# Performance work log

Measured on AMD Instinct MI355X. Metric: run time of the kernel, lower is better.

The kernel has to match this reference:

```python
import jax, jax.numpy as jnp
import numpy as np

D = 128        # d_model
VOCAB = 2000   # vocab_size
NUM_ITERS = 6
NUM_V = 98304  # total vertices = 3 * num_edges
NUM_E = NUM_V // 3


def setup_inputs() -> dict:
    key = jax.random.key(0)
    ks = jax.random.split(key, 20)
    std = 0.02
    inp = {
        "x_v": jax.random.randint(ks[0], (NUM_V,), 0, VOCAB),
        "target_mask": jax.random.randint(ks[1], (NUM_V,), 0, 2) > 0,
        # embedding table (vocab_size + 1 rows, last is padding idx)
        "emb": jax.random.normal(ks[2], (VOCAB + 1, D), jnp.float32) * std,
        # edge_init: Linear(1, d_model)
        "edge_init_w": jax.random.normal(ks[3], (D, 1), jnp.float32) * std,
        "edge_init_b": jnp.zeros((D,), jnp.float32),
        # vertex_to_edge LSTM(3d -> d): torch gate order i,f,g,o
        "Wih_v2e": jax.random.normal(ks[4], (4 * D, 3 * D), jnp.float32) * (1.0 / np.sqrt(D)),
        "Whh_v2e": jax.random.normal(ks[5], (4 * D, D), jnp.float32) * (1.0 / np.sqrt(D)),
        "bih_v2e": jax.random.normal(ks[6], (4 * D,), jnp.float32) * (1.0 / np.sqrt(D)),
        "bhh_v2e": jax.random.normal(ks[7], (4 * D,), jnp.float32) * (1.0 / np.sqrt(D)),
        # edge_to_vertex: 3 position-specific LSTM(d -> d), stacked along axis 0
        "Wih_e2v": jax.random.normal(ks[8], (3, 4 * D, D), jnp.float32) * (1.0 / np.sqrt(D)),
        "Whh_e2v": jax.random.normal(ks[9], (3, 4 * D, D), jnp.float32) * (1.0 / np.sqrt(D)),
        "bih_e2v": jax.random.normal(ks[10], (3, 4 * D), jnp.float32) * (1.0 / np.sqrt(D)),
        "bhh_e2v": jax.random.normal(ks[11], (3, 4 * D), jnp.float32) * (1.0 / np.sqrt(D)),
        # output projection Linear(d -> vocab)
        "out_w": jax.random.normal(ks[12], (VOCAB, D), jnp.float32) * std,
        "out_b": jnp.zeros((VOCAB,), jnp.float32),
    }
    return inp


def _lstm_cell(gates, c):
    # torch LSTM gate order: input, forget, cell(g), output
    i, f, g, o = jnp.split(gates, 4, axis=-1)
    c_new = jax.nn.sigmoid(f) * c + jax.nn.sigmoid(i) * jnp.tanh(g)
    h_new = jax.nn.sigmoid(o) * jnp.tanh(c_new)
    return h_new, c_new


def reference(x_v, target_mask, emb, edge_init_w, edge_init_b,
              Wih_v2e, Whh_v2e, bih_v2e, bhh_v2e,
              Wih_e2v, Whh_e2v, bih_e2v, bhh_e2v,
              out_w, out_b):
    E = x_v.shape[0] // 3
    # init embeddings (-1 ids would map to padding row VOCAB; ids are in-range here)
    h_v = emb[x_v].reshape(E, 3, D)              # [E, 3, D]
    c_v = jnp.zeros_like(h_v)
    h_e = jnp.broadcast_to(edge_init_w[:, 0] + edge_init_b, (E, D))  # Linear(1->D) on ones
    c_e = jnp.zeros_like(h_e)
    mask = target_mask.reshape(E, 3)[..., None]  # [E, 3, 1]
    b_v2e = bih_v2e + bhh_v2e                    # [4D]
    b_e2v = (bih_e2v + bhh_e2v)[None]            # [1, 3, 4D]

    for _ in range(NUM_ITERS):
        # vertex -> edge: concat 3 vertices, one LSTM cell step
        msg = h_v.reshape(E, 3 * D)
        gates_e = msg @ Wih_v2e.T + h_e @ Whh_v2e.T + b_v2e          # [E, 4D]
        h_e, c_e = _lstm_cell(gates_e, c_e)
        # edge -> vertex: 3 position-specific LSTM cells, same edge input
        gates_v = (jnp.einsum('ed,pkd->epk', h_e, Wih_e2v)
                   + jnp.einsum('epd,pkd->epk', h_v, Whh_e2v)
                   + b_e2v)                                          # [E, 3, 4D]
        h_new, c_new = _lstm_cell(gates_v, c_v)
        h_v = jnp.where(mask, h_new, h_v)
        c_v = jnp.where(mask, c_new, c_v)

    logits = h_v.reshape(3 * E, D) @ out_w.T + out_b                 # [3E, VOCAB]
    return logits
```

## Files before the change

kernel.cpp:

```cpp
#include <hip/hip_runtime.h>

#define E_CNT 32768
#define V_CNT 98304
#define D_ 128
#define VOCAB_ 2000
#define ITERS_ 6

typedef unsigned short u16;
typedef _Float16 f16;
typedef __attribute__((ext_vector_type(8))) _Float16 f16x8;
typedef __attribute__((ext_vector_type(4))) float f32x4;

__device__ __forceinline__ f32x4 MFh(f16x8 a, f16x8 b, f32x4 c) {
    return __builtin_amdgcn_mfma_f32_16x16x32_f16(a, b, c, 0, 0, 0);
}
__device__ __forceinline__ float sigmoid_f(float x) {
    return __builtin_amdgcn_rcpf(1.0f + __expf(-x));
}
__device__ __forceinline__ float tanh_f(float x) {
    float ax = fabsf(x);
    float t = fmaf(-2.0f, __builtin_amdgcn_rcpf(__expf(2.0f * ax) + 1.0f), 1.0f);
    return copysignf(t, x);
}

__global__ void detect_mask_kernel(const unsigned int* __restrict__ m, int* __restrict__ flag) {
    int i = blockIdx.x * 256 + threadIdx.x;
    if (i < 4096 && m[i] > 1u) atomicOr(flag, 1);
}

__global__ void prep_kernel(
    const float* __restrict__ Wih_v2e, const float* __restrict__ Whh_v2e,
    const float* __restrict__ bih_v2e, const float* __restrict__ bhh_v2e,
    const float* __restrict__ Wih_e2v, const float* __restrict__ Whh_e2v,
    const float* __restrict__ bih_e2v, const float* __restrict__ bhh_e2v,
    const float* __restrict__ out_w,
    f16* __restrict__ WvF, f16* __restrict__ WeF, f16* __restrict__ OwF,
    float* __restrict__ bv, float* __restrict__ be)
{
    int idx = blockIdx.x * 256 + threadIdx.x;
    if (idx < 262144) {
        const int r = idx & 7, l = (idx >> 3) & 63, t = idx >> 9;
        const int kk = t & 15, nt = t >> 4;
        const int j = nt * 16 + (l & 15);
        const int k = kk * 32 + (l >> 4) * 8 + r;
        const float w = (k < 384) ? Wih_v2e[j * 384 + k] : Whh_v2e[j * 128 + (k - 384)];
        WvF[idx] = (f16)w;
        return;
    }
    idx -= 262144;
    if (idx < 393216) {
        const int r = idx & 7, l = (idx >> 3) & 63, t = idx >> 9;
        const int kk = t & 7, nt = (t >> 3) & 31, p = t >> 8;
        const int j = nt * 16 + (l & 15);
        const int k = kk * 32 + (l >> 4) * 8 + r;
        const float w = (k < 128) ? Wih_e2v[(p * 512 + j) * 128 + k]
                                  : Whh_e2v[(p * 512 + j) * 128 + (k - 128)];
        WeF[idx] = (f16)w;
        return;
    }
    idx -= 393216;
    if (idx < 256000) {
        const int r = idx & 7, l = (idx >> 3) & 63, t = idx >> 9;
        const int kk = t & 3, nt = t >> 2;
        const int j = nt * 16 + (l & 15);
        const int k = kk * 32 + (l >> 4) * 8 + r;
        OwF[idx] = (f16)out_w[j * 128 + k];
        return;
    }
    idx -= 256000;
    if (idx < 512) { bv[idx] = bih_v2e[idx] + bhh_v2e[idx]; return; }
    idx -= 512;
    if (idx < 1536) { be[idx] = bih_e2v[idx] + bhh_e2v[idx]; return; }
}

__global__ __launch_bounds__(512)
void fused_kernel(
    const int* __restrict__ x_v,
    const float* __restrict__ emb,
    const float* __restrict__ eiw, const float* __restrict__ eib,
    const f16* __restrict__ WvF, const f16* __restrict__ WeF,
    const float* __restrict__ bv, const float* __restrict__ be,
    const void* __restrict__ mask, const int* __restrict__ flagp,
    float4* __restrict__ cvG4,
    f16* __restrict__ hvOut)
{
    __shared__ f16 HV[24576];
    __shared__ f16 HE[8192];

    const int tid = threadIdx.x;
    const int c = tid >> 6, l = tid & 63;
    const int lr = l & 15, lk = l >> 4;
    const int e0 = blockIdx.x * 64;

    for (int i = tid; i < 64 * 48; i += 512) {
        const int row = i / 48, seg = i % 48;
        int id = x_v[(e0 + row) * 3 + (seg >> 4)];
        if (id < 0 || id > VOCAB_) id = VOCAB_;
        const float* s = emb + id * D_ + ((seg * 8) & 127);
        float4 a = *(const float4*)s, b = *(const float4*)(s + 4);
        f16x8 H;
        H[0] = (f16)a.x; H[1] = (f16)a.y; H[2] = (f16)a.z; H[3] = (f16)a.w;
        H[4] = (f16)b.x; H[5] = (f16)b.y; H[6] = (f16)b.z; H[7] = (f16)b.w;
        *(f16x8*)&HV[((row >> 4) * 12 + (seg >> 2)) * 512 + (seg & 3) * 128 + (row & 15) * 8] = H;
    }
    for (int i = tid; i < 64 * 16; i += 512) {
        const int row = i / 16, seg = i % 16;
        f16x8 H;
        #pragma unroll
        for (int j = 0; j < 8; ++j) H[j] = (f16)(eiw[seg * 8 + j] + eib[seg * 8 + j]);
        *(f16x8*)&HE[((row >> 4) * 4 + (seg >> 2)) * 512 + (seg & 3) * 128 + (row & 15) * 8] = H;
    }

    const int isByte = *flagp;
    unsigned mbits[3];
    #pragma unroll
    for (int p = 0; p < 3; ++p) {
        unsigned mb = 0;
        #pragma unroll
        for (int mt = 0; mt < 4; ++mt)
            #pragma unroll
            for (int r = 0; r < 4; ++r) {
                const int v = (e0 + mt * 16 + lk * 4 + r) * 3 + p;
                const bool m = isByte ? (((const unsigned char*)mask)[v] != 0)
                                      : (((const int*)mask)[v] != 0);
                mb |= (unsigned)m << (mt * 4 + r);
            }
        mbits[p] = mb;
    }
    const int d = c * 16 + lr;
    const int wBase = (c >> 1) * 512 + ((c & 1) * 2 + (lr >> 3)) * 128 + lk * 32 + (lr & 7);
    float ce[4][4];
    #pragma unroll
    for (int mt = 0; mt < 4; ++mt)
        #pragma unroll
        for (int r = 0; r < 4; ++r) ce[mt][r] = 0.0f;

    __syncthreads();

    const f16* HVl = HV + l * 8;
    const f16* HEl = HE + l * 8;
    const size_t cvBase = (size_t)blockIdx.x * 12 * 512 + tid;

    #pragma unroll 1
    for (int it = 0; it < ITERS_; ++it) {
        {
            f32x4 acc[4][4];
            #pragma unroll
            for (int mt = 0; mt < 4; ++mt)
                #pragma unroll
                for (int g = 0; g < 4; ++g) acc[mt][g] = (f32x4)0.0f;

            #pragma unroll 2
            for (int kk = 0; kk < 16; ++kk) {
                f16x8 Ah[4];
                if (kk < 12) {
                    #pragma unroll
                    for (int mt = 0; mt < 4; ++mt)
                        Ah[mt] = *(const f16x8*)(HVl + (mt * 12 + kk) * 512);
                } else {
                    #pragma unroll
                    for (int mt = 0; mt < 4; ++mt)
                        Ah[mt] = *(const f16x8*)(HEl + (mt * 4 + (kk - 12)) * 512);
                }
                #pragma unroll
                for (int g = 0; g < 4; ++g) {
                    f16x8 B = *(const f16x8*)(WvF + (((g * 8 + c) * 16 + kk) * 64 + l) * 8);
                    #pragma unroll
                    for (int mt = 0; mt < 4; ++mt)
                        acc[mt][g] = MFh(Ah[mt], B, acc[mt][g]);
                }
            }
            __syncthreads();
            const float bvi = bv[d], bvf = bv[128 + d], bvg = bv[256 + d], bvo = bv[384 + d];
            #pragma unroll
            for (int mt = 0; mt < 4; ++mt)
                #pragma unroll
                for (int r = 0; r < 4; ++r) {
                    float gi = sigmoid_f(acc[mt][0][r] + bvi);
                    float gf = sigmoid_f(acc[mt][1][r] + bvf);
                    float gg = tanh_f(acc[mt][2][r] + bvg);
                    float go = sigmoid_f(acc[mt][3][r] + bvo);
                    float cn = gf * ce[mt][r] + gi * gg;
                    ce[mt][r] = cn;
                    HE[wBase + mt * 2048 + r * 8] = (f16)(go * tanh_f(cn));
                }
            __syncthreads();
        }
        #pragma unroll 1
        for (int p = 0; p < 3; ++p) {
            f32x4 acc[4][4];
            #pragma unroll
            for (int mt = 0; mt < 4; ++mt)
                #pragma unroll
                for (int g = 0; g < 4; ++g) acc[mt][g] = (f32x4)0.0f;

            #pragma unroll 2
            for (int kk = 0; kk < 8; ++kk) {
                f16x8 Ah[4];
                if (kk < 4) {
                    #pragma unroll
                    for (int mt = 0; mt < 4; ++mt)
                        Ah[mt] = *(const f16x8*)(HEl + (mt * 4 + kk) * 512);
                } else {
                    #pragma unroll
                    for (int mt = 0; mt < 4; ++mt)
                        Ah[mt] = *(const f16x8*)(HVl + (mt * 12 + p * 4 + (kk - 4)) * 512);
                }
                #pragma unroll
                for (int g = 0; g < 4; ++g) {
                    f16x8 B = *(const f16x8*)(WeF + ((((p * 32) + (g * 8 + c)) * 8 + kk) * 64 + l) * 8);
                    #pragma unroll
                    for (int mt = 0; mt < 4; ++mt)
                        acc[mt][g] = MFh(Ah[mt], B, acc[mt][g]);
                }
            }
            __syncthreads();
            const float bei = be[p * 512 + d], bef = be[p * 512 + 128 + d];
            const float beg = be[p * 512 + 256 + d], beo = be[p * 512 + 384 + d];
            #pragma unroll
            for (int mt = 0; mt < 4; ++mt) {
                const size_t ci = cvBase + (p * 4 + mt) * 512;
                float cvv[4] = {0.0f, 0.0f, 0.0f, 0.0f};
                if (it > 0) {
                    float4 t = cvG4[ci];
                    cvv[0] = t.x; cvv[1] = t.y; cvv[2] = t.z; cvv[3] = t.w;
                }
                #pragma unroll
                for (int r = 0; r < 4; ++r) {
                    if ((mbits[p] >> (mt * 4 + r)) & 1u) {
                        float gi = sigmoid_f(acc[mt][0][r] + bei);
                        float gf = sigmoid_f(acc[mt][1][r] + bef);
                        float gg = tanh_f(acc[mt][2][r] + beg);
                        float go = sigmoid_f(acc[mt][3][r] + beo);
                        float cn = gf * cvv[r] + gi * gg;
                        cvv[r] = cn;
                        HV[wBase + mt * 6144 + p * 2048 + r * 8] = (f16)(go * tanh_f(cn));
                    }
                }
                cvG4[ci] = make_float4(cvv[0], cvv[1], cvv[2], cvv[3]);
            }
        }
        __syncthreads();
    }

    for (int i = tid; i < 64 * 48; i += 512) {
        const int row = i / 48, seg = i % 48;
        *(f16x8*)&hvOut[(size_t)(e0 + row) * 384 + seg * 8] =
            *(const f16x8*)&HV[((row >> 4) * 12 + (seg >> 2)) * 512 + (seg & 3) * 128 + (row & 15) * 8];
    }
}

__global__ __launch_bounds__(256) void proj_kernel(
    const f16* __restrict__ hv, const f16* __restrict__ WF,
    const float* __restrict__ out_b, float* __restrict__ out)
{
    __shared__ char occ_pad[49152];
    const int tid = threadIdx.x, l = tid & 63;
    occ_pad[tid] = (char)tid;
    __syncthreads();
    {
        int keep = (int)occ_pad[(tid + 1) & 255];
        asm volatile("" :: "v"(keep));
    }

    const int wid = blockIdx.x * 4 + (tid >> 6);
    const int v0 = wid * 32;
    const int lr = l & 15, lk = l >> 4;

    f16x8 Bv[2][4];
    #pragma unroll
    for (int vt = 0; vt < 2; ++vt)
        #pragma unroll
        for (int kk = 0; kk < 4; ++kk)
            Bv[vt][kk] = *(const f16x8*)(hv + (v0 + vt * 16 + lr) * D_ + kk * 32 + lk * 8);

    f16x8 Wc[4];
    #pragma unroll
    for (int kk = 0; kk < 4; ++kk)
        Wc[kk] = *(const f16x8*)(WF + (kk * 64 + l) * 8);

    #pragma unroll 2
    for (int nt = 0; nt < 125; ++nt) {
        f16x8 Wn[4];
        if (nt < 124) {
            #pragma unroll
            for (int kk = 0; kk < 4; ++kk)
                Wn[kk] = *(const f16x8*)(WF + (((nt + 1) * 4 + kk) * 64 + l) * 8);
        }
        f32x4 a0 = (f32x4)0.0f, a1 = (f32x4)0.0f;
        #pragma unroll
        for (int kk = 0; kk < 4; ++kk) {
            a0 = MFh(Wc[kk], Bv[0][kk], a0);
            a1 = MFh(Wc[kk], Bv[1][kk], a1);
        }
        const int n0 = nt * 16 + lk * 4;
        const float4 bb = *(const float4*)&out_b[n0];
        {
            const size_t v = (size_t)(v0 + lr);
            float4 o = make_float4(a0[0] + bb.x, a0[1] + bb.y, a0[2] + bb.z, a0[3] + bb.w);
            *(float4*)&out[v * VOCAB_ + n0] = o;
        }
        {
            const size_t v = (size_t)(v0 + 16 + lr);
            float4 o = make_float4(a1[0] + bb.x, a1[1] + bb.y, a1[2] + bb.z, a1[3] + bb.w);
            *(float4*)&out[v * VOCAB_ + n0] = o;
        }
        #pragma unroll
        for (int q = 0; q < 4; ++q) Wc[q] = Wn[q];
    }
}

extern "C" void kernel_launch(void* const* d_in, const int* in_sizes, int n_in,
                              void* d_out, int out_size, void* d_ws, size_t ws_size,
                              hipStream_t stream)
{
    const int*   x_v     = (const int*)  d_in[0];
    const void*  mask    = d_in[1];
    const float* emb     = (const float*)d_in[2];
    const float* eiw     = (const float*)d_in[3];
    const float* eib     = (const float*)d_in[4];
    const float* Wih_v2e = (const float*)d_in[5];
    const float* Whh_v2e = (const float*)d_in[6];
    const float* bih_v2e = (const float*)d_in[7];
    const float* bhh_v2e = (const float*)d_in[8];
    const float* Wih_e2v = (const float*)d_in[9];
    const float* Whh_e2v = (const float*)d_in[10];
    const float* bih_e2v = (const float*)d_in[11];
    const float* bhh_e2v = (const float*)d_in[12];
    const float* out_w   = (const float*)d_in[13];
    const float* out_b   = (const float*)d_in[14];
    float* out = (float*)d_out;

    char* ws = (char*)d_ws;
    f16*    hv   = (f16*)(ws);
    f16*    WvF  = (f16*)(ws + 25165824);
    f16*    WeF  = (f16*)(ws + 25690112);
    f16*    OwF  = (f16*)(ws + 26476544);
    float*  bv   = (float*)(ws + 26988544);
    float*  be   = (float*)(ws + 26990592);
    int*    flag = (int*)(ws + 26996736);
    float4* cvG4 = (float4*)(ws + 27000832);

    hipMemsetAsync(flag, 0, 4, stream);
    detect_mask_kernel<<<16, 256, 0, stream>>>((const unsigned int*)mask, flag);
    prep_kernel<<<3568, 256, 0, stream>>>(Wih_v2e, Whh_v2e, bih_v2e, bhh_v2e,
                                          Wih_e2v, Whh_e2v, bih_e2v, bhh_e2v, out_w,
                                          WvF, WeF, OwF, bv, be);
    fused_kernel<<<E_CNT / 64, 512, 0, stream>>>(x_v, emb, eiw, eib,
                                                 WvF, WeF, bv, be,
                                                 mask, flag, cvG4, hv);
    proj_kernel<<<V_CNT / 128, 256, 0, stream>>>(hv, OwF, out_b, out);
}
```

Baseline: 794.0 us.

## Double-buffer edge hidden state and batch vertex writes to cut block barriers

Splits the edge hidden-state buffer into two ping-pong shared buffers so the v2e epilogue can write h_e without the barrier that used to follow its GEMM. The three e2v position writes to HV are held in registers and committed after a single barrier, replacing one barrier per position. It also raises wave priority around the MFMA loops. The trade-offs are more registers for the held outputs, extra dynamic shared memory that may lower occupancy, and gate math computed for every lane instead of only masked ones.

```diff
diff --git a/kernel.cpp b/kernel.cpp
--- a/kernel.cpp
+++ b/kernel.cpp
@@ -7,6 +7,7 @@
 #define ITERS_ 6
 
 typedef unsigned short u16;
+typedef unsigned int u32;
 typedef _Float16 f16;
 typedef __attribute__((ext_vector_type(8))) _Float16 f16x8;
 typedef __attribute__((ext_vector_type(4))) float f32x4;
@@ -21,6 +22,12 @@
     float ax = fabsf(x);
     float t = fmaf(-2.0f, __builtin_amdgcn_rcpf(__expf(2.0f * ax) + 1.0f), 1.0f);
     return copysignf(t, x);
+}
+__device__ __forceinline__ u16 f16bits(f16 h) {
+    union { f16 f; u16 u; } cv; cv.f = h; return cv.u;
+}
+__device__ __forceinline__ f16 bits2f16(u16 u) {
+    union { f16 f; u16 u; } cv; cv.u = u; return cv.f;
 }
 
 __global__ void detect_mask_kernel(const unsigned int* __restrict__ m, int* __restrict__ flag) {
@@ -85,7 +92,8 @@
     f16* __restrict__ hvOut)
 {
     __shared__ f16 HV[24576];
-    __shared__ f16 HE[8192];
+    __shared__ f16 HEa[8192];
+    extern __shared__ f16 HEb[];
 
     const int tid = threadIdx.x;
     const int c = tid >> 6, l = tid & 63;
@@ -108,7 +116,7 @@
         f16x8 H;
         #pragma unroll
         for (int j = 0; j < 8; ++j) H[j] = (f16)(eiw[seg * 8 + j] + eib[seg * 8 + j]);
-        *(f16x8*)&HE[((row >> 4) * 4 + (seg >> 2)) * 512 + (seg & 3) * 128 + (row & 15) * 8] = H;
+        *(f16x8*)&HEa[((row >> 4) * 4 + (seg >> 2)) * 512 + (seg & 3) * 128 + (row & 15) * 8] = H;
     }
 
     const int isByte = *flagp;
@@ -138,11 +146,14 @@
     __syncthreads();
 
     const f16* HVl = HV + l * 8;
-    const f16* HEl = HE + l * 8;
     const size_t cvBase = (size_t)blockIdx.x * 12 * 512 + tid;
 
     #pragma unroll 1
     for (int it = 0; it < ITERS_; ++it) {
+        const f16* HErd = (it & 1) ? HEb : HEa;
+        f16*       HEwr = (it & 1) ? HEa : HEb;
+        const f16* HErdl = HErd + l * 8;
+
         {
             f32x4 acc[4][4];
             #pragma unroll
@@ -150,6 +161,7 @@
                 #pragma unroll
                 for (int g = 0; g < 4; ++g) acc[mt][g] = (f32x4)0.0f;
 
+            __builtin_amdgcn_s_setprio(1);
             #pragma unroll 2
             for (int kk = 0; kk < 16; ++kk) {
                 f16x8 Ah[4];
@@ -160,7 +172,7 @@
                 } else {
                     #pragma unroll
                     for (int mt = 0; mt < 4; ++mt)
-                        Ah[mt] = *(const f16x8*)(HEl + (mt * 4 + (kk - 12)) * 512);
+                        Ah[mt] = *(const f16x8*)(HErdl + (mt * 4 + (kk - 12)) * 512);
                 }
                 #pragma unroll
                 for (int g = 0; g < 4; ++g) {
@@ -170,7 +182,8 @@
                         acc[mt][g] = MFh(Ah[mt], B, acc[mt][g]);
                 }
             }
-            __syncthreads();
+            __builtin_amdgcn_s_setprio(0);
+
             const float bvi = bv[d], bvf = bv[128 + d], bvg = bv[256 + d], bvo = bv[384 + d];
             #pragma unroll
             for (int mt = 0; mt < 4; ++mt)
@@ -182,10 +195,13 @@
                     float go = sigmoid_f(acc[mt][3][r] + bvo);
                     float cn = gf * ce[mt][r] + gi * gg;
                     ce[mt][r] = cn;
-                    HE[wBase + mt * 2048 + r * 8] = (f16)(go * tanh_f(cn));
-                }
-            __syncthreads();
-        }
+                    HEwr[wBase + mt * 2048 + r * 8] = (f16)(go * tanh_f(cn));
+                }
+        }
+        __syncthreads();
+
+        const f16* HEwrl = HEwr + l * 8;
+        u32 hold[3][4][2];
         #pragma unroll 1
         for (int p = 0; p < 3; ++p) {
             f32x4 acc[4][4];
@@ -194,13 +210,14 @@
                 #pragma unroll
                 for (int g = 0; g < 4; ++g) acc[mt][g] = (f32x4)0.0f;
 
+            __builtin_amdgcn_s_setprio(1);
             #pragma unroll 2
             for (int kk = 0; kk < 8; ++kk) {
                 f16x8 Ah[4];
                 if (kk < 4) {
                     #pragma unroll
                     for (int mt = 0; mt < 4; ++mt)
-                        Ah[mt] = *(const f16x8*)(HEl + (mt * 4 + kk) * 512);
+                        Ah[mt] = *(const f16x8*)(HEwrl + (mt * 4 + kk) * 512);
                 } else {
                     #pragma unroll
                     for (int mt = 0; mt < 4; ++mt)
@@ -214,7 +231,8 @@
                         acc[mt][g] = MFh(Ah[mt], B, acc[mt][g]);
                 }
             }
-            __syncthreads();
+            __builtin_amdgcn_s_setprio(0);
+
             const float bei = be[p * 512 + d], bef = be[p * 512 + 128 + d];
             const float beg = be[p * 512 + 256 + d], beo = be[p * 512 + 384 + d];
             #pragma unroll
@@ -225,21 +243,37 @@
                     float4 t = cvG4[ci];
                     cvv[0] = t.x; cvv[1] = t.y; cvv[2] = t.z; cvv[3] = t.w;
                 }
+                u16 hb[4];
+                #pragma unroll
+                for (int r = 0; r < 4; ++r) {
+                    float gi = sigmoid_f(acc[mt][0][r] + bei);
+                    float gf = sigmoid_f(acc[mt][1][r] + bef);
+                    float gg = tanh_f(acc[mt][2][r] + beg);
+                    float go = sigmoid_f(acc[mt][3][r] + beo);
+                    float cn = gf * cvv[r] + gi * gg;
+                    const bool m = (mbits[p] >> (mt * 4 + r)) & 1u;
+                    if (m) cvv[r] = cn;
+                    hb[r] = f16bits((f16)(go * tanh_f(cn)));
+                }
+                cvG4[ci] = make_float4(cvv[0], cvv[1], cvv[2], cvv[3]);
+                hold[p][mt][0] = (u32)hb[0] | ((u32)hb[1] << 16);
+                hold[p][mt][1] = (u32)hb[2] | ((u32)hb[3] << 16);
+            }
+        }
+        __syncthreads();
+
+        #pragma unroll
+        for (int p = 0; p < 3; ++p)
+            #pragma unroll
+            for (int mt = 0; mt < 4; ++mt)
                 #pragma unroll
                 for (int r = 0; r < 4; ++r) {
                     if ((mbits[p] >> (mt * 4 + r)) & 1u) {
-                        float gi = sigmoid_f(acc[mt][0][r] + bei);
-                        float gf = sigmoid_f(acc[mt][1][r] + bef);
-                        float gg = tanh_f(acc[mt][2][r] + beg);
-                        float go = sigmoid_f(acc[mt][3][r] + beo);
-                        float cn = gf * cvv[r] + gi * gg;
-                        cvv[r] = cn;
-                        HV[wBase + mt * 6144 + p * 2048 + r * 8] = (f16)(go * tanh_f(cn));
+                        u32 w = hold[p][mt][r >> 1];
+                        u16 hb = (r & 1) ? (u16)(w >> 16) : (u16)(w & 0xFFFF);
+                        HV[wBase + mt * 6144 + p * 2048 + r * 8] = bits2f16(hb);
                     }
                 }
-                cvG4[ci] = make_float4(cvv[0], cvv[1], cvv[2], cvv[3]);
-            }
-        }
         __syncthreads();
     }
 
@@ -341,13 +375,16 @@
     int*    flag = (int*)(ws + 26996736);
     float4* cvG4 = (float4*)(ws + 27000832);
 
+    hipFuncSetAttribute(reinterpret_cast<const void*>(fused_kernel),
+                        hipFuncAttributeMaxDynamicSharedMemorySize, 16384);
+
     hipMemsetAsync(flag, 0, 4, stream);
     detect_mask_kernel<<<16, 256, 0, stream>>>((const unsigned int*)mask, flag);
     prep_kernel<<<3568, 256, 0, stream>>>(Wih_v2e, Whh_v2e, bih_v2e, bhh_v2e,
                                           Wih_e2v, Whh_e2v, bih_e2v, bhh_e2v, out_w,
                                           WvF, WeF, OwF, bv, be);
-    fused_kernel<<<E_CNT / 64, 512, 0, stream>>>(x_v, emb, eiw, eib,
-                                                 WvF, WeF, bv, be,
-                                                 mask, flag, cvG4, hv);
+    fused_kernel<<<E_CNT / 64, 512, 16384, stream>>>(x_v, emb, eiw, eib,
+                                                     WvF, WeF, bv, be,
+                                                     mask, flag, cvG4, hv);
     proj_kernel<<<V_CNT / 128, 256, 0, stream>>>(hv, OwF, out_b, out);
 }
```

Result: slower. 1.025 ms (+29.1%).
